# Performance work log

Measured on AMD Instinct MI355X. Metric: run time of the kernel, lower is better.

Reference implementation:

```python
import jax, jax.numpy as jnp
import numpy as np

D = 2048; Nl = 2; Nh = 32; Nkv = 8; V = 32000; Dh = 5632; Lm = 4096
B = 1; L = 2048; E = 1e-5
DHEAD = D // Nh  # 64


def setup_inputs() -> dict:
    key = jax.random.key(0)
    ks = jax.random.split(key, 10)
    s = 0.02
    rn = lambda k, shape: jax.random.normal(k, shape, jnp.float32) * s
    emb = rn(ks[0], (V, D))
    wq = rn(ks[1], (Nl, D, D))
    wk = rn(ks[2], (Nl, D, D * Nkv // Nh))
    wv = rn(ks[3], (Nl, D, D * Nkv // Nh))
    wa = rn(ks[4], (Nl, D, D))
    wg = rn(ks[5], (Nl, D, Dh))
    wu = rn(ks[6], (Nl, D, Dh))
    wd = rn(ks[7], (Nl, Dh, D))
    w_an = jnp.ones((Nl, D), jnp.float32)
    w_fn = jnp.ones((Nl, D), jnp.float32)
    w_on = jnp.ones((D,), jnp.float32)
    w_out = rn(ks[8], (D, V))
    # RoPE tables (interleaved-pair convention, matching reshape(..., -1, 2))
    theta = 1.0 / (10000.0 ** (jnp.arange(0, DHEAD, 2, dtype=jnp.float32) / DHEAD))
    freqs = jnp.outer(jnp.arange(Lm, dtype=jnp.float32), theta)  # [Lm, DHEAD//2]
    cos = jnp.cos(freqs)
    sin = jnp.sin(freqs)
    ti = jax.random.randint(ks[9], (B, L), 0, V)
    return dict(ti=ti, emb=emb, wq=wq, wk=wk, wv=wv, wa=wa, w_an=w_an, w_fn=w_fn,
                wg=wg, wu=wu, wd=wd, w_on=w_on, w_out=w_out, cos=cos, sin=sin)


def _rmsnorm(x, w):
    return x * jax.lax.rsqrt(jnp.mean(x * x, -1, keepdims=True) + E) * w


def _rope(x, cos, sin):
    # x: [B, L, H, DHEAD]; cos/sin: [1, L, 1, DHEAD//2]; interleaved pairs
    xs = x.reshape(*x.shape[:-1], DHEAD // 2, 2)
    xr, xi = xs[..., 0], xs[..., 1]
    r1 = xr * cos - xi * sin
    i1 = xr * sin + xi * cos
    return jnp.stack([r1, i1], axis=-1).reshape(x.shape)


def reference(ti, emb, wq, wk, wv, wa, w_an, w_fn, wg, wu, wd, w_on, w_out, cos, sin):
    cos_l = cos[:L].reshape(1, L, 1, DHEAD // 2)
    sin_l = sin[:L].reshape(1, L, 1, DHEAD // 2)
    mask = jnp.triu(jnp.full((1, 1, L, L), -jnp.inf, jnp.float32), 1)
    scale = 1.0 / jnp.sqrt(jnp.float32(DHEAD))
    rep = Nh // Nkv
    x = emb[ti]  # [B, L, D]
    for l in range(Nl):
        h = _rmsnorm(x, w_an[l])
        q = (h @ wq[l]).reshape(B, L, Nh, DHEAD)
        k = (h @ wk[l]).reshape(B, L, Nkv, DHEAD)
        v = (h @ wv[l]).reshape(B, L, Nkv, DHEAD)
        q = _rope(q, cos_l, sin_l)
        k = _rope(k, cos_l, sin_l)
        kx = jnp.repeat(k, rep, axis=2)  # GQA expand -> [B, L, Nh, DHEAD]
        vx = jnp.repeat(v, rep, axis=2)
        a = jnp.einsum('blhd,bmhd->bhlm', q, kx) * scale
        p = jax.nn.softmax(a + mask, axis=-1)
        sa = jnp.einsum('bhlm,bmhd->blhd', p, vx).reshape(B, L, D)
        x = x + sa @ wa[l]
        hf = _rmsnorm(x, w_fn[l])
        x = x + (jax.nn.silu(hf @ wg[l]) * (hf @ wu[l])) @ wd[l]
    return _rmsnorm(x, w_on) @ w_out  # [B, L, V]
```

## Files before the change

### kernel.cpp

```cpp
#include <hip/hip_runtime.h>
#include <hip/hip_bf16.h>

#define DMODEL 2048
#define LSEQ   2048
#define NHEAD  32
#define NKVH   8
#define DHEAD  64
#define DFF    5632
#define VOCAB  32000

typedef __attribute__((ext_vector_type(8))) short bf16x8;
typedef __attribute__((ext_vector_type(4))) float f32x4;
typedef __attribute__((ext_vector_type(8))) unsigned short ushort8;

__device__ __forceinline__ void gload_lds16(const __hip_bfloat16* g, __hip_bfloat16* l) {
  __builtin_amdgcn_global_load_lds((const void __attribute__((address_space(1)))*)g,
                                   (void __attribute__((address_space(3)))*)l, 16, 0, 0);
}

__device__ __forceinline__ float bfbits2f(unsigned short u) {
  return __uint_as_float(((unsigned int)u) << 16);
}
__device__ __forceinline__ unsigned short f2bfbits(float f) {
  unsigned int x = __float_as_uint(f);
  return (unsigned short)((x + 0x7fffu + ((x >> 16) & 1u)) >> 16);
}

__global__ __launch_bounds__(256) void embed_k(const int* __restrict__ ti,
                                               const float* __restrict__ emb,
                                               float* __restrict__ x) {
  const int row = blockIdx.x;
  const int t = threadIdx.x;
  const int tok = ti[row];
  const float4* s = (const float4*)(emb + (size_t)tok * DMODEL);
  float4* d = (float4*)(x + (size_t)row * DMODEL);
  d[t] = s[t];
  d[t + 256] = s[t + 256];
}

__global__ __launch_bounds__(256) void rmsnorm_k(const float* __restrict__ x,
                                                 const float* __restrict__ w,
                                                 __hip_bfloat16* __restrict__ out) {
  const int row = blockIdx.x;
  const int t = threadIdx.x;
  const float4* xr = (const float4*)(x + (size_t)row * DMODEL);
  float4 a = xr[t];
  float4 b = xr[t + 256];
  float ss = a.x*a.x + a.y*a.y + a.z*a.z + a.w*a.w
           + b.x*b.x + b.y*b.y + b.z*b.z + b.w*b.w;
  #pragma unroll
  for (int m = 32; m >= 1; m >>= 1) ss += __shfl_xor(ss, m);
  __shared__ float red[4];
  if ((t & 63) == 0) red[t >> 6] = ss;
  __syncthreads();
  const float tot = red[0] + red[1] + red[2] + red[3];
  const float sc = rsqrtf(tot * (1.0f / DMODEL) + 1e-5f);
  const float4* w4 = (const float4*)w;
  float4 wa_ = w4[t], wb_ = w4[t + 256];
  __hip_bfloat16* o = out + (size_t)row * DMODEL;
  o[4*t + 0] = __float2bfloat16(a.x * sc * wa_.x);
  o[4*t + 1] = __float2bfloat16(a.y * sc * wa_.y);
  o[4*t + 2] = __float2bfloat16(a.z * sc * wa_.z);
  o[4*t + 3] = __float2bfloat16(a.w * sc * wa_.w);
  o[1024 + 4*t + 0] = __float2bfloat16(b.x * sc * wb_.x);
  o[1024 + 4*t + 1] = __float2bfloat16(b.y * sc * wb_.y);
  o[1024 + 4*t + 2] = __float2bfloat16(b.z * sc * wb_.z);
  o[1024 + 4*t + 3] = __float2bfloat16(b.w * sc * wb_.w);
}

__global__ __launch_bounds__(256) void transpose_k(const float* __restrict__ src,
                                                   __hip_bfloat16* __restrict__ dst,
                                                   int K, int N) {
  __shared__ float tile[64 * 65];
  const int kb = blockIdx.x * 64;
  const int nb = blockIdx.y * 64;
  const int t = threadIdx.x;
  #pragma unroll
  for (int i = 0; i < 16; ++i) {
    const int idx = t + 256 * i;
    const int r = idx >> 6, c = idx & 63;
    tile[r * 65 + c] = src[(size_t)(kb + r) * N + nb + c];
  }
  __syncthreads();
  #pragma unroll
  for (int i = 0; i < 16; ++i) {
    const int idx = t + 256 * i;
    const int n = idx >> 6, k = idx & 63;
    dst[(size_t)(nb + n) * K + kb + k] = __float2bfloat16(tile[k * 65 + n]);
  }
}

template <int EPI>
__global__ __launch_bounds__(256) void gemm_bt(const __hip_bfloat16* __restrict__ A,
                                               const __hip_bfloat16* __restrict__ Bt,
                                               float* __restrict__ Cf,
                                               __hip_bfloat16* __restrict__ Cb,
                                               int M, int N, int K) {
  __shared__ __align__(16) __hip_bfloat16 As[128 * 32];
  __shared__ __align__(16) __hip_bfloat16 Bs[128 * 32];
  const int tid = threadIdx.x;
  const int wave = tid >> 6;
  const int lane = tid & 63;
  const int nbx = M >> 7;
  const int nwg = nbx * (N >> 7);
  const int orig = blockIdx.y * nbx + blockIdx.x;
  const int wid = (orig & 7) * (nwg >> 3) + (orig >> 3);
  const int tm = (wid % nbx) << 7;
  const int tn = (wid / nbx) << 7;
  const int wr = (wave >> 1) * 64;
  const int wc = (wave & 1) * 64;
  const int fr = lane & 15;
  const int fg = lane >> 4;
  const f32x4 fzero = {0.f, 0.f, 0.f, 0.f};
  f32x4 acc[4][4];
  #pragma unroll
  for (int i = 0; i < 4; ++i)
    #pragma unroll
    for (int j = 0; j < 4; ++j) acc[i][j] = fzero;
  const int srow = wave * 32 + (lane >> 2);
  const int scol = (lane & 3) * 8;
  const __hip_bfloat16* gA = A + (size_t)(tm + srow) * K + scol;
  const __hip_bfloat16* gB = Bt + (size_t)(tn + srow) * K + scol;
  __hip_bfloat16* lA = &As[wave * 1024];
  __hip_bfloat16* lB = &Bs[wave * 1024];
  for (int k0 = 0; k0 < K; k0 += 32) {
    gload_lds16(gA, lA);
    gload_lds16(gA + (size_t)16 * K, lA + 512);
    gload_lds16(gB, lB);
    gload_lds16(gB + (size_t)16 * K, lB + 512);
    gA += 32; gB += 32;
    __syncthreads();
    bf16x8 af[4], bfr[4];
    #pragma unroll
    for (int i = 0; i < 4; ++i) af[i] = *(const bf16x8*)&As[(wr + i * 16 + fr) * 32 + fg * 8];
    #pragma unroll
    for (int j = 0; j < 4; ++j) bfr[j] = *(const bf16x8*)&Bs[(wc + j * 16 + fr) * 32 + fg * 8];
    #pragma unroll
    for (int i = 0; i < 4; ++i)
      #pragma unroll
      for (int j = 0; j < 4; ++j)
        acc[i][j] = __builtin_amdgcn_mfma_f32_16x16x32_bf16(af[i], bfr[j], acc[i][j], 0, 0, 0);
    __syncthreads();
  }
  #pragma unroll
  for (int i = 0; i < 4; ++i)
    #pragma unroll
    for (int j = 0; j < 4; ++j)
      #pragma unroll
      for (int r = 0; r < 4; ++r) {
        const int row = tm + wr + i * 16 + fg * 4 + r;
        const int col = tn + wc + j * 16 + fr;
        const float v = acc[i][j][r];
        if (EPI == 0) Cf[(size_t)row * N + col] = v;
        else if (EPI == 1) Cb[(size_t)row * N + col] = __float2bfloat16(v);
        else Cf[(size_t)row * N + col] += v;
      }
}

template <int EPI>
__global__ __launch_bounds__(512, 2) void gemm8p(const __hip_bfloat16* __restrict__ A,
                                                 const __hip_bfloat16* __restrict__ Bt,
                                                 float* __restrict__ Cf,
                                                 __hip_bfloat16* __restrict__ Cb,
                                                 int M, int N, int K) {
  __shared__ __align__(16) __hip_bfloat16 lds[2][2][256 * 64];
  const int tid = threadIdx.x;
  const int wave = tid >> 6;
  const int lane = tid & 63;
  const int nbx = M >> 8;
  const int nwg = nbx * (N >> 8);
  const int orig = blockIdx.y * nbx + blockIdx.x;
  const int wid = (orig & 7) * (nwg >> 3) + (orig >> 3);
  const int tm = (wid % nbx) << 8;
  const int tn = (wid / nbx) << 8;
  const int wm = wave >> 2;
  const int wn = wave & 3;
  const int fr = lane & 15;
  const int fg = lane >> 4;
  const int l3 = lane >> 3;
  const int l7 = lane & 7;
  const int swzcol = (l3 ^ l7) << 3;
  const size_t sK = (size_t)K;

  const __hip_bfloat16* pA = A + (size_t)(tm + wave * 8 + l3) * sK + swzcol;
  const __hip_bfloat16* pB = Bt + (size_t)(tn + wave * 8 + l3) * sK + swzcol;

#define STAGE8(buf) do {                                                          \
    _Pragma("unroll")                                                             \
    for (int i_ = 0; i_ < 4; ++i_) {                                              \
      gload_lds16(pA + (size_t)(i_ * 64) * sK, &lds[buf][0][(i_ * 64 + wave * 8) * 64]); \
      gload_lds16(pB + (size_t)(i_ * 64) * sK, &lds[buf][1][(i_ * 64 + wave * 8) * 64]); \
    }                                                                             \
    pA += 64; pB += 64;                                                           \
  } while (0)

  const int NT = K >> 6;
  STAGE8(0);
  STAGE8(1);

  const f32x4 fzero = {0.f, 0.f, 0.f, 0.f};
  f32x4 acc[8][4];
  #pragma unroll
  for (int i = 0; i < 8; ++i)
    #pragma unroll
    for (int j = 0; j < 4; ++j) acc[i][j] = fzero;

  const int wmo = wm * 128;
  const int wno = wn * 64;
  const int rswz = (fr & 7) << 4;
  const int ct0 = ((fg * 16) ^ rswz) >> 1;
  const int ct1 = ((64 + fg * 16) ^ rswz) >> 1;

  int cur = 0;
  for (int kt = 0; kt < NT; ++kt) {
    if (kt + 1 < NT) { asm volatile("s_waitcnt vmcnt(8)" ::: "memory"); }
    else             { asm volatile("s_waitcnt vmcnt(0)" ::: "memory"); }
    __builtin_amdgcn_s_barrier();
    __builtin_amdgcn_sched_barrier(0);
    const __hip_bfloat16* LA = &lds[cur][0][0];
    const __hip_bfloat16* LB = &lds[cur][1][0];
    #pragma unroll
    for (int q = 0; q < 4; ++q) {
      const int mb = (q & 1) * 4;
      const int nb = (q >> 1) * 2;
      bf16x8 av[4][2], bv[2][2];
      #pragma unroll
      for (int mi = 0; mi < 4; ++mi) {
        av[mi][0] = *(const bf16x8*)&LA[(wmo + (mb + mi) * 16 + fr) * 64 + ct0];
        av[mi][1] = *(const bf16x8*)&LA[(wmo + (mb + mi) * 16 + fr) * 64 + ct1];
      }
      #pragma unroll
      for (int ni = 0; ni < 2; ++ni) {
        bv[ni][0] = *(const bf16x8*)&LB[(wno + (nb + ni) * 16 + fr) * 64 + ct0];
        bv[ni][1] = *(const bf16x8*)&LB[(wno + (nb + ni) * 16 + fr) * 64 + ct1];
      }
      __builtin_amdgcn_s_setprio(1);
      #pragma unroll
      for (int mi = 0; mi < 4; ++mi)
        #pragma unroll
        for (int ni = 0; ni < 2; ++ni) {
          acc[mb + mi][nb + ni] = __builtin_amdgcn_mfma_f32_16x16x32_bf16(
              av[mi][0], bv[ni][0], acc[mb + mi][nb + ni], 0, 0, 0);
          acc[mb + mi][nb + ni] = __builtin_amdgcn_mfma_f32_16x16x32_bf16(
              av[mi][1], bv[ni][1], acc[mb + mi][nb + ni], 0, 0, 0);
        }
      __builtin_amdgcn_s_setprio(0);
      __builtin_amdgcn_s_barrier();
    }
    __builtin_amdgcn_sched_barrier(0);
    if (kt + 2 < NT) { STAGE8(cur); }
    cur ^= 1;
  }
#undef STAGE8
  #pragma unroll
  for (int mf = 0; mf < 8; ++mf)
    #pragma unroll
    for (int nf = 0; nf < 4; ++nf)
      #pragma unroll
      for (int r = 0; r < 4; ++r) {
        const int row = tm + wmo + mf * 16 + fg * 4 + r;
        const int col = tn + wno + nf * 16 + fr;
        const float v = acc[mf][nf][r];
        if (EPI == 0) Cf[(size_t)row * N + col] = v;
        else if (EPI == 1) Cb[(size_t)row * N + col] = __float2bfloat16(v);
        else Cf[(size_t)row * N + col] += v;
      }
}

__global__ __launch_bounds__(256) void rope_k(__hip_bfloat16* __restrict__ qkv,
                                              const float* __restrict__ cosT,
                                              const float* __restrict__ sinT) {
  const int row = blockIdx.x;
  const int t = threadIdx.x;
  unsigned int* base = (unsigned int*)(qkv + (size_t)row * 3072);
  #pragma unroll
  for (int p = t; p < 1280; p += 256) {
    const int hp = p >> 5;
    const int i = p & 31;
    const unsigned int packed = base[hp * 32 + i];
    const float x0 = bfbits2f((unsigned short)(packed & 0xffffu));
    const float x1 = bfbits2f((unsigned short)(packed >> 16));
    const float c = cosT[row * 32 + i];
    const float s = sinT[row * 32 + i];
    const float r0 = x0 * c - x1 * s;
    const float r1 = x0 * s + x1 * c;
    base[hp * 32 + i] = (unsigned int)f2bfbits(r0) | ((unsigned int)f2bfbits(r1) << 16);
  }
}

__global__ __launch_bounds__(256) void attn_k(const __hip_bfloat16* __restrict__ qkv,
                                              __hip_bfloat16* __restrict__ out) {
  const int h = blockIdx.x;
  const int qt = blockIdx.y;
  const int tid = threadIdx.x;
  const int wave = tid >> 6;
  const int lane = tid & 63;
  const int fr = lane & 15;
  const int fg = lane >> 4;
  const int qb = qt * 64;
  const int kcol = DMODEL + (h >> 2) * DHEAD;
  const int vcol = DMODEL + NKVH * DHEAD + (h >> 2) * DHEAD;
  __shared__ __align__(16) __hip_bfloat16 Ks[64 * 72];
  __shared__ __align__(16) __hip_bfloat16 Vt[64 * 72];
  __shared__ __align__(16) __hip_bfloat16 Ps[4][16 * 72];
  bf16x8 qf[2];
  {
    const __hip_bfloat16* qp = qkv + (size_t)(qb + wave * 16 + fr) * 3072 + h * DHEAD + fg * 8;
    qf[0] = *(const bf16x8*)qp;
    qf[1] = *(const bf16x8*)(qp + 32);
  }
  const f32x4 fzero = {0.f, 0.f, 0.f, 0.f};
  float m_run[4], l_run[4];
  f32x4 o[4];
  #pragma unroll
  for (int r = 0; r < 4; ++r) { m_run[r] = -1e30f; l_run[r] = 0.f; }
  #pragma unroll
  for (int c = 0; c < 4; ++c) o[c] = fzero;

  const int sr = tid >> 2;
  const int sc = (tid & 3) * 16;
  for (int t = 0; t <= qt; ++t) {
    const __hip_bfloat16* kp = qkv + (size_t)(t * 64 + sr) * 3072 + kcol + sc;
    *(float4*)&Ks[sr * 72 + sc] = *(const float4*)kp;
    *(float4*)&Ks[sr * 72 + sc + 8] = *(const float4*)(kp + 8);
    const __hip_bfloat16* vp = qkv + (size_t)(t * 64 + sr) * 3072 + vcol + sc;
    ushort8 v0 = *(const ushort8*)vp;
    ushort8 v1 = *(const ushort8*)(vp + 8);
    unsigned short* vt = (unsigned short*)Vt;
    #pragma unroll
    for (int i = 0; i < 8; ++i) {
      vt[(sc + i) * 72 + sr] = v0[i];
      vt[(sc + 8 + i) * 72 + sr] = v1[i];
    }
    __syncthreads();
    f32x4 s[4];
    #pragma unroll
    for (int c = 0; c < 4; ++c) {
      s[c] = fzero;
      #pragma unroll
      for (int ks = 0; ks < 2; ++ks) {
        bf16x8 kf = *(const bf16x8*)&Ks[(c * 16 + fr) * 72 + ks * 32 + fg * 8];
        s[c] = __builtin_amdgcn_mfma_f32_16x16x32_bf16(qf[ks], kf, s[c], 0, 0, 0);
      }
    }
    const int rowg = qb + wave * 16 + fg * 4;
    #pragma unroll
    for (int c = 0; c < 4; ++c)
      #pragma unroll
      for (int r = 0; r < 4; ++r) {
        float v = s[c][r] * 0.125f;
        if (t * 64 + c * 16 + fr > rowg + r) v = -1e30f;
        s[c][r] = v;
      }
    #pragma unroll
    for (int r = 0; r < 4; ++r) {
      float pm = fmaxf(fmaxf(s[0][r], s[1][r]), fmaxf(s[2][r], s[3][r]));
      pm = fmaxf(pm, __shfl_xor(pm, 1));
      pm = fmaxf(pm, __shfl_xor(pm, 2));
      pm = fmaxf(pm, __shfl_xor(pm, 4));
      pm = fmaxf(pm, __shfl_xor(pm, 8));
      const float mn = fmaxf(m_run[r], pm);
      const float al = __expf(m_run[r] - mn);
      m_run[r] = mn;
      float rs = 0.f;
      #pragma unroll
      for (int c = 0; c < 4; ++c) { float p = __expf(s[c][r] - mn); s[c][r] = p; rs += p; }
      rs += __shfl_xor(rs, 1);
      rs += __shfl_xor(rs, 2);
      rs += __shfl_xor(rs, 4);
      rs += __shfl_xor(rs, 8);
      l_run[r] = l_run[r] * al + rs;
      #pragma unroll
      for (int c = 0; c < 4; ++c) o[c][r] *= al;
    }
    unsigned short* pw = (unsigned short*)Ps[wave];
    #pragma unroll
    for (int c = 0; c < 4; ++c)
      #pragma unroll
      for (int r = 0; r < 4; ++r)
        pw[(fg * 4 + r) * 72 + c * 16 + fr] = f2bfbits(s[c][r]);
    #pragma unroll
    for (int ks = 0; ks < 2; ++ks) {
      bf16x8 pf = *(const bf16x8*)&Ps[wave][fr * 72 + ks * 32 + fg * 8];
      #pragma unroll
      for (int c = 0; c < 4; ++c) {
        bf16x8 vf = *(const bf16x8*)&Vt[(c * 16 + fr) * 72 + ks * 32 + fg * 8];
        o[c] = __builtin_amdgcn_mfma_f32_16x16x32_bf16(pf, vf, o[c], 0, 0, 0);
      }
    }
    __syncthreads();
  }
  #pragma unroll
  for (int c = 0; c < 4; ++c)
    #pragma unroll
    for (int r = 0; r < 4; ++r)
      out[(size_t)(qb + wave * 16 + fg * 4 + r) * DMODEL + h * DHEAD + c * 16 + fr] =
          __float2bfloat16(o[c][r] / l_run[r]);
}

__global__ __launch_bounds__(256) void silu_k(const __hip_bfloat16* __restrict__ gu,
                                              __hip_bfloat16* __restrict__ mb) {
  const int row = blockIdx.x;
  const int t = threadIdx.x;
  const ushort8* g8 = (const ushort8*)(gu + (size_t)row * (2 * DFF));
  const ushort8* u8 = (const ushort8*)(gu + (size_t)row * (2 * DFF) + DFF);
  ushort8* m8 = (ushort8*)(mb + (size_t)row * DFF);
  for (int j = t; j * 8 < DFF; j += 256) {
    ushort8 g = g8[j], u = u8[j];
    ushort8 ov;
    #pragma unroll
    for (int i = 0; i < 8; ++i) {
      const float gf = bfbits2f(g[i]);
      const float uf = bfbits2f(u[i]);
      ov[i] = f2bfbits(gf / (1.f + __expf(-gf)) * uf);
    }
    m8[j] = ov;
  }
}

extern "C" void kernel_launch(void* const* d_in, const int* in_sizes, int n_in,
                              void* d_out, int out_size, void* d_ws, size_t ws_size,
                              hipStream_t stream) {
  const int* ti = (const int*)d_in[0];
  const float* emb = (const float*)d_in[1];
  const float* wq = (const float*)d_in[2];
  const float* wk = (const float*)d_in[3];
  const float* wv = (const float*)d_in[4];
  const float* wa = (const float*)d_in[5];
  const float* w_an = (const float*)d_in[6];
  const float* w_fn = (const float*)d_in[7];
  const float* wg = (const float*)d_in[8];
  const float* wu = (const float*)d_in[9];
  const float* wd = (const float*)d_in[10];
  const float* w_on = (const float*)d_in[11];
  const float* w_out = (const float*)d_in[12];
  const float* cosT = (const float*)d_in[13];
  const float* sinT = (const float*)d_in[14];
  float* outp = (float*)d_out;

  char* ws = (char*)d_ws;
  float* x            = (float*)(ws + 0);
  __hip_bfloat16* h   = (__hip_bfloat16*)(ws + 16777216);
  __hip_bfloat16* qkv = (__hip_bfloat16*)(ws + 25165824);
  __hip_bfloat16* att = (__hip_bfloat16*)(ws + 37748736);
  __hip_bfloat16* gu  = (__hip_bfloat16*)(ws + 46137344);
  __hip_bfloat16* mb  = (__hip_bfloat16*)(ws + 92274688);
  __hip_bfloat16* wTqkv = (__hip_bfloat16*)(ws + 115343360);
  __hip_bfloat16* wTa   = (__hip_bfloat16*)(ws + 127926272);
  __hip_bfloat16* wTgu  = (__hip_bfloat16*)(ws + 136314880);
  __hip_bfloat16* wTd   = (__hip_bfloat16*)(ws + 182452224);
  __hip_bfloat16* wTout = (__hip_bfloat16*)(ws + 25165824);
  (void)in_sizes; (void)n_in; (void)out_size; (void)ws_size;

  const dim3 blk(256);
  embed_k<<<2048, blk, 0, stream>>>(ti, emb, x);
  for (int l = 0; l < 2; ++l) {
    transpose_k<<<dim3(32, 32), blk, 0, stream>>>(wq + (size_t)l * 2048 * 2048, wTqkv, 2048, 2048);
    transpose_k<<<dim3(32, 8),  blk, 0, stream>>>(wk + (size_t)l * 2048 * 512, wTqkv + (size_t)2048 * 2048, 2048, 512);
    transpose_k<<<dim3(32, 8),  blk, 0, stream>>>(wv + (size_t)l * 2048 * 512, wTqkv + (size_t)2560 * 2048, 2048, 512);
    transpose_k<<<dim3(32, 32), blk, 0, stream>>>(wa + (size_t)l * 2048 * 2048, wTa, 2048, 2048);
    transpose_k<<<dim3(32, 88), blk, 0, stream>>>(wg + (size_t)l * 2048 * 5632, wTgu, 2048, 5632);
    transpose_k<<<dim3(32, 88), blk, 0, stream>>>(wu + (size_t)l * 2048 * 5632, wTgu + (size_t)5632 * 2048, 2048, 5632);
    transpose_k<<<dim3(88, 32), blk, 0, stream>>>(wd + (size_t)l * 5632 * 2048, wTd, 5632, 2048);

    rmsnorm_k<<<2048, blk, 0, stream>>>(x, w_an + l * 2048, h);
    gemm_bt<1><<<dim3(16, 24), blk, 0, stream>>>(h, wTqkv, nullptr, qkv, 2048, 3072, 2048);
    rope_k<<<2048, blk, 0, stream>>>(qkv, cosT, sinT);
    attn_k<<<dim3(32, 32), blk, 0, stream>>>(qkv, att);
    gemm_bt<2><<<dim3(16, 16), blk, 0, stream>>>(att, wTa, x, nullptr, 2048, 2048, 2048);

    rmsnorm_k<<<2048, blk, 0, stream>>>(x, w_fn + l * 2048, h);
    gemm8p<1><<<dim3(8, 44), dim3(512), 0, stream>>>(h, wTgu, nullptr, gu, 2048, 11264, 2048);
    silu_k<<<2048, blk, 0, stream>>>(gu, mb);
    gemm_bt<2><<<dim3(16, 16), blk, 0, stream>>>(mb, wTd, x, nullptr, 2048, 2048, 5632);
  }
  transpose_k<<<dim3(32, 500), blk, 0, stream>>>(w_out, wTout, 2048, 32000);
  rmsnorm_k<<<2048, blk, 0, stream>>>(x, w_on, h);
  gemm8p<0><<<dim3(8, 125), dim3(512), 0, stream>>>(h, wTout, outp, nullptr, 2048, 32000, 2048);
}
```

Measured before the change: 1.583 ms.

## Load full LDS tile into registers up front and interleave prefetch with MFMAs

The GEMM main loop now reads every A/B fragment for the current k-tile from LDS into registers at once. It then issues the next-next tile's global-to-LDS loads interleaved with the four MFMA groups. This replaces the per-quadrant barriers and the separate staging phase after compute, so each k-step has fewer barriers and global loads overlap the matrix math. The cost is more live VGPRs for fragments (8x2 + 4x2 bf16x8), which may hurt occupancy or cause spills.

```diff
diff --git a/kernel.cpp b/kernel.cpp
--- a/kernel.cpp
+++ b/kernel.cpp
@@ -185,18 +185,18 @@
   const __hip_bfloat16* pA = A + (size_t)(tm + wave * 8 + l3) * sK + swzcol;
   const __hip_bfloat16* pB = Bt + (size_t)(tn + wave * 8 + l3) * sK + swzcol;
 
-#define STAGE8(buf) do {                                                          \
-    _Pragma("unroll")                                                             \
-    for (int i_ = 0; i_ < 4; ++i_) {                                              \
-      gload_lds16(pA + (size_t)(i_ * 64) * sK, &lds[buf][0][(i_ * 64 + wave * 8) * 64]); \
-      gload_lds16(pB + (size_t)(i_ * 64) * sK, &lds[buf][1][(i_ * 64 + wave * 8) * 64]); \
-    }                                                                             \
-    pA += 64; pB += 64;                                                           \
-  } while (0)
-
-  const int NT = K >> 6;
-  STAGE8(0);
-  STAGE8(1);
+  #pragma unroll
+  for (int j = 0; j < 4; ++j) {
+    gload_lds16(pA + (size_t)(j * 64) * sK, &lds[0][0][(j * 64 + wave * 8) * 64]);
+    gload_lds16(pB + (size_t)(j * 64) * sK, &lds[0][1][(j * 64 + wave * 8) * 64]);
+  }
+  pA += 64; pB += 64;
+  #pragma unroll
+  for (int j = 0; j < 4; ++j) {
+    gload_lds16(pA + (size_t)(j * 64) * sK, &lds[1][0][(j * 64 + wave * 8) * 64]);
+    gload_lds16(pB + (size_t)(j * 64) * sK, &lds[1][1][(j * 64 + wave * 8) * 64]);
+  }
+  pA += 64; pB += 64;
 
   const f32x4 fzero = {0.f, 0.f, 0.f, 0.f};
   f32x4 acc[8][4];
@@ -211,47 +211,59 @@
   const int ct0 = ((fg * 16) ^ rswz) >> 1;
   const int ct1 = ((64 + fg * 16) ^ rswz) >> 1;
 
-  int cur = 0;
+  asm volatile("s_waitcnt vmcnt(8)" ::: "memory");
+  __builtin_amdgcn_s_barrier();
+  __builtin_amdgcn_sched_barrier(0);
+
+  const int NT = K >> 6;
   for (int kt = 0; kt < NT; ++kt) {
-    if (kt + 1 < NT) { asm volatile("s_waitcnt vmcnt(8)" ::: "memory"); }
-    else             { asm volatile("s_waitcnt vmcnt(0)" ::: "memory"); }
+    const int cur = kt & 1;
+    const __hip_bfloat16* LA = &lds[cur][0][0];
+    const __hip_bfloat16* LB = &lds[cur][1][0];
+    bf16x8 av[8][2], bv[4][2];
+    #pragma unroll
+    for (int mi = 0; mi < 8; ++mi) {
+      av[mi][0] = *(const bf16x8*)&LA[(wmo + mi * 16 + fr) * 64 + ct0];
+      av[mi][1] = *(const bf16x8*)&LA[(wmo + mi * 16 + fr) * 64 + ct1];
+    }
+    #pragma unroll
+    for (int ni = 0; ni < 4; ++ni) {
+      bv[ni][0] = *(const bf16x8*)&LB[(wno + ni * 16 + fr) * 64 + ct0];
+      bv[ni][1] = *(const bf16x8*)&LB[(wno + ni * 16 + fr) * 64 + ct1];
+    }
+    asm volatile("s_waitcnt lgkmcnt(0)" ::: "memory");
+    __builtin_amdgcn_sched_barrier(0);
     __builtin_amdgcn_s_barrier();
     __builtin_amdgcn_sched_barrier(0);
-    const __hip_bfloat16* LA = &lds[cur][0][0];
-    const __hip_bfloat16* LB = &lds[cur][1][0];
+    const bool pre = (kt + 2 < NT);
     #pragma unroll
     for (int q = 0; q < 4; ++q) {
+      if (pre) {
+        gload_lds16(pA + (size_t)(q * 64) * sK, &lds[cur][0][(q * 64 + wave * 8) * 64]);
+        gload_lds16(pB + (size_t)(q * 64) * sK, &lds[cur][1][(q * 64 + wave * 8) * 64]);
+      }
       const int mb = (q & 1) * 4;
       const int nb = (q >> 1) * 2;
-      bf16x8 av[4][2], bv[2][2];
-      #pragma unroll
-      for (int mi = 0; mi < 4; ++mi) {
-        av[mi][0] = *(const bf16x8*)&LA[(wmo + (mb + mi) * 16 + fr) * 64 + ct0];
-        av[mi][1] = *(const bf16x8*)&LA[(wmo + (mb + mi) * 16 + fr) * 64 + ct1];
-      }
-      #pragma unroll
-      for (int ni = 0; ni < 2; ++ni) {
-        bv[ni][0] = *(const bf16x8*)&LB[(wno + (nb + ni) * 16 + fr) * 64 + ct0];
-        bv[ni][1] = *(const bf16x8*)&LB[(wno + (nb + ni) * 16 + fr) * 64 + ct1];
-      }
       __builtin_amdgcn_s_setprio(1);
       #pragma unroll
       for (int mi = 0; mi < 4; ++mi)
         #pragma unroll
         for (int ni = 0; ni < 2; ++ni) {
           acc[mb + mi][nb + ni] = __builtin_amdgcn_mfma_f32_16x16x32_bf16(
-              av[mi][0], bv[ni][0], acc[mb + mi][nb + ni], 0, 0, 0);
+              av[mb + mi][0], bv[nb + ni][0], acc[mb + mi][nb + ni], 0, 0, 0);
           acc[mb + mi][nb + ni] = __builtin_amdgcn_mfma_f32_16x16x32_bf16(
-              av[mi][1], bv[ni][1], acc[mb + mi][nb + ni], 0, 0, 0);
+              av[mb + mi][1], bv[nb + ni][1], acc[mb + mi][nb + ni], 0, 0, 0);
         }
       __builtin_amdgcn_s_setprio(0);
+    }
+    if (pre) { pA += 64; pB += 64; }
+    if (kt + 1 < NT) {
+      if (pre) asm volatile("s_waitcnt vmcnt(8)" ::: "memory");
+      else     asm volatile("s_waitcnt vmcnt(0)" ::: "memory");
       __builtin_amdgcn_s_barrier();
-    }
-    __builtin_amdgcn_sched_barrier(0);
-    if (kt + 2 < NT) { STAGE8(cur); }
-    cur ^= 1;
-  }
-#undef STAGE8
+      __builtin_amdgcn_sched_barrier(0);
+    }
+  }
   #pragma unroll
   for (int mf = 0; mf < 8; ++mf)
     #pragma unroll
```

Result: faster. 1.469 ms (-7.2%).
